# Performance work log

Measured on AMD Instinct MI355X. Metric: run time of the kernel, lower is better.

The kernel has to match this reference:

```python
import jax, jax.numpy as jnp
import numpy as np

S, V, E, H = 4096, 10000, 128, 256
NE, TK, NH, HD, FF, NL = 4, 2, 4, 64, 2048, 2
EPS = 1e-5
SCALE = 1.0 / np.sqrt(HD).astype(np.float32)


def setup_inputs() -> dict:
    key = jax.random.key(0)
    ks = iter(jax.random.split(key, 64))
    n = lambda shape: jax.random.normal(next(ks), shape, jnp.float32) * 0.02
    inp = {"x": jax.random.randint(next(ks), (S,), 0, V)}
    inp["emb"] = n((V, E))
    for i, din in enumerate([E, H, H]):
        inp[f"moe{i}_gw"] = n((NE, din))
        inp[f"moe{i}_gb"] = jnp.zeros((NE,), jnp.float32)
        inp[f"moe{i}_ew"] = n((NE, H, din))
        inp[f"moe{i}_eb"] = jnp.zeros((NE, H), jnp.float32)
    inp["attn_in_w"] = n((NL, 3 * H, H)); inp["attn_in_b"] = jnp.zeros((NL, 3 * H), jnp.float32)
    inp["attn_out_w"] = n((NL, H, H));    inp["attn_out_b"] = jnp.zeros((NL, H), jnp.float32)
    inp["ln1_g"] = jnp.ones((NL, H), jnp.float32); inp["ln1_b"] = jnp.zeros((NL, H), jnp.float32)
    inp["ln2_g"] = jnp.ones((NL, H), jnp.float32); inp["ln2_b"] = jnp.zeros((NL, H), jnp.float32)
    inp["ff1_w"] = n((NL, FF, H)); inp["ff1_b"] = jnp.zeros((NL, FF), jnp.float32)
    inp["ff2_w"] = n((NL, H, FF)); inp["ff2_b"] = jnp.zeros((NL, H), jnp.float32)
    inp["fc_w"] = n((H, H)); inp["fc_b"] = jnp.zeros((H,), jnp.float32)
    inp["out_w"] = n((V, H)); inp["out_b"] = jnp.zeros((V,), jnp.float32)
    return inp


def _ln(x, g, b):
    m = x.mean(-1, keepdims=True)
    v = ((x - m) ** 2).mean(-1, keepdims=True)
    return (x - m) * jax.lax.rsqrt(v + EPS) * g + b


def _moe(x, gw, gb, ew, eb):
    # x: [S, din]. Faithful quirk: experts are the top-k of TOKEN 0's gates,
    # applied to every token, weighted by each token's own top-k gate scores.
    scores = jax.nn.softmax(x @ gw.T + gb, axis=-1)            # [S, NE]
    vals, idx = jax.lax.top_k(scores, TK)                      # [S, TK]
    sel = idx[0]                                               # [TK]
    outs = jnp.einsum('si,khi->skh', x, ew[sel]) + eb[sel][None]  # [S, TK, H]
    return (outs * vals[:, :, None]).sum(axis=1)               # [S, H]


def reference(x, emb,
              moe0_gw, moe0_gb, moe0_ew, moe0_eb,
              moe1_gw, moe1_gb, moe1_ew, moe1_eb,
              moe2_gw, moe2_gb, moe2_ew, moe2_eb,
              attn_in_w, attn_in_b, attn_out_w, attn_out_b,
              ln1_g, ln1_b, ln2_g, ln2_b,
              ff1_w, ff1_b, ff2_w, ff2_b,
              fc_w, fc_b, out_w, out_b):
    h = emb[x]                                                 # [S, E]
    for gw, gb, ew, eb in [(moe0_gw, moe0_gb, moe0_ew, moe0_eb),
                           (moe1_gw, moe1_gb, moe1_ew, moe1_eb),
                           (moe2_gw, moe2_gb, moe2_ew, moe2_eb)]:
        h = _moe(h, gw, gb, ew, eb)                            # [S, H]
    for l in range(NL):  # post-norm TransformerEncoderLayer (relu, no dropout at eval)
        qkv = h @ attn_in_w[l].T + attn_in_b[l]                # [S, 3H]
        q, k, v = [t.reshape(S, NH, HD) for t in jnp.split(qkv, 3, axis=-1)]
        att = jax.nn.softmax(jnp.einsum('shd,thd->hst', q, k) * SCALE, axis=-1)
        a = jnp.einsum('hst,thd->shd', att, v).reshape(S, H)
        h = _ln(h + a @ attn_out_w[l].T + attn_out_b[l], ln1_g[l], ln1_b[l])
        ffh = jax.nn.relu(h @ ff1_w[l].T + ff1_b[l]) @ ff2_w[l].T + ff2_b[l]
        h = _ln(h + ffh, ln2_g[l], ln2_b[l])
    h = h @ fc_w.T + fc_b                                      # [S, H]
    logits = h @ out_w.T + out_b                               # [S, V]
    return jax.nn.log_softmax(logits, axis=-1)
```

## Files before the change

### kernel.cpp

```cpp
#include <hip/hip_runtime.h>
#include <math.h>

#define S_ 4096
#define V_ 10000
#define E_ 128
#define H_ 256
#define NE_ 4
#define NH_ 4
#define HD_ 64
#define FF_ 2048
#define NL_ 2
#define EPS_ 1e-5f
#define SCALE_ 0.125f
#define SPLITS_ 4
#define PSTRIDE_ 160

typedef __attribute__((ext_vector_type(8))) short bf16x8;
typedef __attribute__((ext_vector_type(4))) float f32x4;

static __device__ __forceinline__ short f2bf(float f) {
  unsigned u = __builtin_bit_cast(unsigned, f);
  unsigned r = (u + 0x7fffu + ((u >> 16) & 1u)) >> 16;
  return (short)r;
}
static __device__ __forceinline__ float bf2f(short s) {
  unsigned u = ((unsigned)(unsigned short)s) << 16;
  return __builtin_bit_cast(float, u);
}

struct CvtArgs {
  const float* src[9];
  short* dst[9];
  int pfx[10];
};
__global__ __launch_bounds__(256) void k_cvt(CvtArgs a, const int* __restrict__ x,
                                             const float* __restrict__ emb,
                                             short* __restrict__ h) {
  int b = blockIdx.x;
  if (b >= a.pfx[9]) {
    int i8 = (b - a.pfx[9]) * 2048 + threadIdx.x * 8;
    int s = i8 >> 7, e = i8 & 127;
    const float* sp = &emb[(size_t)x[s] * E_ + e];
    float4 v0 = *(const float4*)sp;
    float4 v1 = *(const float4*)(sp + 4);
    short4 o0, o1;
    o0.x = f2bf(v0.x); o0.y = f2bf(v0.y); o0.z = f2bf(v0.z); o0.w = f2bf(v0.w);
    o1.x = f2bf(v1.x); o1.y = f2bf(v1.y); o1.z = f2bf(v1.z); o1.w = f2bf(v1.w);
    *(short4*)&h[i8] = o0;
    *(short4*)&h[i8 + 4] = o1;
    return;
  }
  int s = 0;
  while (b >= a.pfx[s + 1]) ++s;
  size_t base = (size_t)(b - a.pfx[s]) * 2048 + threadIdx.x * 8;
  const float* sp = a.src[s] + base;
  short* dp = a.dst[s] + base;
  float4 v0 = *(const float4*)sp;
  float4 v1 = *(const float4*)(sp + 4);
  short4 o0, o1;
  o0.x = f2bf(v0.x); o0.y = f2bf(v0.y); o0.z = f2bf(v0.z); o0.w = f2bf(v0.w);
  o1.x = f2bf(v1.x); o1.y = f2bf(v1.y); o1.z = f2bf(v1.z); o1.w = f2bf(v1.w);
  *(short4*)dp = o0;
  *(short4*)(dp + 4) = o1;
}

template <int ACT>
__global__ __launch_bounds__(256) void k_gemm64(const short* __restrict__ A,
                                                const short* __restrict__ W,
                                                const float* __restrict__ bias,
                                                short* __restrict__ C,
                                                int M, int N, int K) {
  __shared__ short As[64][72];
  __shared__ short Bs[64][72];
  int bm = blockIdx.y * 64, bn = blockIdx.x * 64;
  int tid = threadIdx.x, lane = tid & 63, wv = tid >> 6;
  int quad = lane >> 4, m16 = lane & 15;
  int wr = (wv >> 1) * 32, wc = (wv & 1) * 32;
  int srow = tid >> 2, scc = (tid & 3) * 16;
  const short* Ar = A + (size_t)(bm + srow) * K + scc;
  const short* Wr = W + (size_t)(bn + srow) * K + scc;
  f32x4 acc[2][2];
#pragma unroll
  for (int m = 0; m < 2; ++m)
#pragma unroll
    for (int n = 0; n < 2; ++n) acc[m][n] = (f32x4){0.f, 0.f, 0.f, 0.f};
  for (int k0 = 0; k0 < K; k0 += 64) {
    *(bf16x8*)&As[srow][scc] = *(const bf16x8*)&Ar[k0];
    *(bf16x8*)&As[srow][scc + 8] = *(const bf16x8*)&Ar[k0 + 8];
    *(bf16x8*)&Bs[srow][scc] = *(const bf16x8*)&Wr[k0];
    *(bf16x8*)&Bs[srow][scc + 8] = *(const bf16x8*)&Wr[k0 + 8];
    __syncthreads();
#pragma unroll
    for (int kk = 0; kk < 2; ++kk) {
      bf16x8 af[2], bf[2];
#pragma unroll
      for (int m = 0; m < 2; ++m) af[m] = *(const bf16x8*)&As[wr + m * 16 + m16][kk * 32 + quad * 8];
#pragma unroll
      for (int n = 0; n < 2; ++n) bf[n] = *(const bf16x8*)&Bs[wc + n * 16 + m16][kk * 32 + quad * 8];
#pragma unroll
      for (int m = 0; m < 2; ++m)
#pragma unroll
        for (int n = 0; n < 2; ++n)
          acc[m][n] = __builtin_amdgcn_mfma_f32_16x16x32_bf16(af[m], bf[n], acc[m][n], 0, 0, 0);
    }
    __syncthreads();
  }
#pragma unroll
  for (int n = 0; n < 2; ++n) {
    int col = bn + wc + n * 16 + m16;
    float b = bias[col];
#pragma unroll
    for (int m = 0; m < 2; ++m) {
      int row0 = bm + wr + m * 16 + quad * 4;
#pragma unroll
      for (int r = 0; r < 4; ++r) {
        float v = acc[m][n][r] + b;
        if (ACT) v = fmaxf(v, 0.f);
        C[(size_t)(row0 + r) * N + col] = f2bf(v);
      }
    }
  }
}

__global__ __launch_bounds__(256) void k_proj(const float* __restrict__ Opart,
                                              const float* __restrict__ Lpart,
                                              const short* __restrict__ W,
                                              const float* __restrict__ bias,
                                              short* __restrict__ C) {
  __shared__ short As[32][40];
  __shared__ short Bs[64][40];
  int bm = blockIdx.y * 32, bn = blockIdx.x * 64;
  int tid = threadIdx.x, lane = tid & 63, wv = tid >> 6;
  int quad = lane >> 4, m16 = lane & 15;
  int wr = (wv >> 1) * 16, wc = (wv & 1) * 32;
  int srow = tid >> 2, sc = (tid & 3) * 8;
  int rowA = bm + (srow & 31);
  const short* Wr = W + (size_t)(bn + srow) * H_ + sc;
  float invden[NH_];
  if (tid < 128) {
#pragma unroll
    for (int hh = 0; hh < NH_; ++hh) {
      float dsum = 0.f;
#pragma unroll
      for (int sp = 0; sp < SPLITS_; ++sp)
        dsum += Lpart[(size_t)(sp * NH_ + hh) * S_ + rowA];
      invden[hh] = 1.0f / dsum;
    }
  }
  f32x4 acc[2];
  acc[0] = (f32x4){0.f, 0.f, 0.f, 0.f};
  acc[1] = (f32x4){0.f, 0.f, 0.f, 0.f};
#pragma unroll
  for (int k0 = 0; k0 < H_; k0 += 32) {
    if (tid < 128) {
      const int head = k0 >> 6;
      int dd = (k0 & 63) + sc;
      float n0 = 0.f, n1 = 0.f, n2 = 0.f, n3 = 0.f, n4 = 0.f, n5 = 0.f, n6 = 0.f, n7 = 0.f;
#pragma unroll
      for (int sp = 0; sp < SPLITS_; ++sp) {
        const float* op = &Opart[((size_t)(sp * NH_ + head) * S_ + rowA) * 64 + dd];
        float4 u0 = *(const float4*)op;
        float4 u1 = *(const float4*)(op + 4);
        n0 += u0.x; n1 += u0.y; n2 += u0.z; n3 += u0.w;
        n4 += u1.x; n5 += u1.y; n6 += u1.z; n7 += u1.w;
      }
      float iv = invden[head];
      union { short s[8]; bf16x8 v; } o;
      o.s[0] = f2bf(n0 * iv); o.s[1] = f2bf(n1 * iv);
      o.s[2] = f2bf(n2 * iv); o.s[3] = f2bf(n3 * iv);
      o.s[4] = f2bf(n4 * iv); o.s[5] = f2bf(n5 * iv);
      o.s[6] = f2bf(n6 * iv); o.s[7] = f2bf(n7 * iv);
      *(bf16x8*)&As[srow][sc] = o.v;
    }
    *(bf16x8*)&Bs[srow][sc] = *(const bf16x8*)&Wr[k0];
    __syncthreads();
    bf16x8 af = *(const bf16x8*)&As[wr + m16][quad * 8];
    bf16x8 bf0 = *(const bf16x8*)&Bs[wc + m16][quad * 8];
    bf16x8 bf1 = *(const bf16x8*)&Bs[wc + 16 + m16][quad * 8];
    acc[0] = __builtin_amdgcn_mfma_f32_16x16x32_bf16(af, bf0, acc[0], 0, 0, 0);
    acc[1] = __builtin_amdgcn_mfma_f32_16x16x32_bf16(af, bf1, acc[1], 0, 0, 0);
    __syncthreads();
  }
#pragma unroll
  for (int n = 0; n < 2; ++n) {
    int col = bn + wc + n * 16 + m16;
    float b = bias[col];
    int row0 = bm + wr + quad * 4;
#pragma unroll
    for (int r = 0; r < 4; ++r) {
      float v = acc[n][r] + b;
      C[(size_t)(row0 + r) * H_ + col] = f2bf(v);
    }
  }
}

__global__ __launch_bounds__(256) void k_ff2(const short* __restrict__ A,
                                             const short* __restrict__ W,
                                             const float* __restrict__ bias,
                                             short* __restrict__ C, int K) {
  __shared__ short As[32][72];
  __shared__ short Bs[64][72];
  int bm = blockIdx.y * 32, bn = blockIdx.x * 64;
  int tid = threadIdx.x, lane = tid & 63, wv = tid >> 6;
  int quad = lane >> 4, m16 = lane & 15;
  int wr = (wv >> 1) * 16, wc = (wv & 1) * 32;
  int arow = tid >> 3, ac = (tid & 7) * 8;
  int brow = tid >> 2, bc = (tid & 3) * 16;
  const short* Ar = A + (size_t)(bm + arow) * K + ac;
  const short* Wr = W + (size_t)(bn + brow) * K + bc;
  f32x4 acc[2];
  acc[0] = (f32x4){0.f, 0.f, 0.f, 0.f};
  acc[1] = (f32x4){0.f, 0.f, 0.f, 0.f};
  for (int k0 = 0; k0 < K; k0 += 64) {
    *(bf16x8*)&As[arow][ac] = *(const bf16x8*)&Ar[k0];
    *(bf16x8*)&Bs[brow][bc] = *(const bf16x8*)&Wr[k0];
    *(bf16x8*)&Bs[brow][bc + 8] = *(const bf16x8*)&Wr[k0 + 8];
    __syncthreads();
    bf16x8 af0 = *(const bf16x8*)&As[wr + m16][quad * 8];
    bf16x8 af1 = *(const bf16x8*)&As[wr + m16][32 + quad * 8];
    bf16x8 b00 = *(const bf16x8*)&Bs[wc + m16][quad * 8];
    bf16x8 b01 = *(const bf16x8*)&Bs[wc + m16][32 + quad * 8];
    bf16x8 b10 = *(const bf16x8*)&Bs[wc + 16 + m16][quad * 8];
    bf16x8 b11 = *(const bf16x8*)&Bs[wc + 16 + m16][32 + quad * 8];
    acc[0] = __builtin_amdgcn_mfma_f32_16x16x32_bf16(af0, b00, acc[0], 0, 0, 0);
    acc[0] = __builtin_amdgcn_mfma_f32_16x16x32_bf16(af1, b01, acc[0], 0, 0, 0);
    acc[1] = __builtin_amdgcn_mfma_f32_16x16x32_bf16(af0, b10, acc[1], 0, 0, 0);
    acc[1] = __builtin_amdgcn_mfma_f32_16x16x32_bf16(af1, b11, acc[1], 0, 0, 0);
    __syncthreads();
  }
#pragma unroll
  for (int n = 0; n < 2; ++n) {
    int col = bn + wc + n * 16 + m16;
    float b = bias[col];
    int row0 = bm + wr + quad * 4;
#pragma unroll
    for (int r = 0; r < 4; ++r) {
      float v = acc[n][r] + b;
      C[(size_t)(row0 + r) * H_ + col] = f2bf(v);
    }
  }
}

__global__ __launch_bounds__(256) void k_moe(const short* __restrict__ A,
                                             const short* __restrict__ EW,
                                             const float* __restrict__ EB,
                                             const float* __restrict__ gw,
                                             const float* __restrict__ gb,
                                             short* __restrict__ C,
                                             int N, int K) {
  __shared__ short As[32][40];
  __shared__ short B0s[64][40];
  __shared__ short B1s[64][40];
  __shared__ float sc_lds[32][NE_];
  __shared__ float g0_lds[NE_];
  __shared__ float vals_lds[32][2];
  __shared__ int sel_lds[2];
  int bm = blockIdx.y * 32, bn = blockIdx.x * 64;
  int tid = threadIdx.x, lane = tid & 63, wv = tid >> 6;
  int quad = lane >> 4, m16 = lane & 15;
  int wr = (wv >> 1) * 16, wc = (wv & 1) * 32;
  int srow = tid >> 2, sc = (tid & 3) * 8;
  if (tid < 128) {
    int r = tid & 31, e = tid >> 5;
    const short* xs = A + (size_t)(bm + r) * K;
    const float* w = gw + (size_t)e * K;
    float acc = 0.f;
    for (int i = 0; i < K; i += 8) {
      bf16x8 xv = *(const bf16x8*)&xs[i];
      float4 w0 = *(const float4*)&w[i];
      float4 w1 = *(const float4*)&w[i + 4];
      acc += bf2f(xv[0]) * w0.x + bf2f(xv[1]) * w0.y + bf2f(xv[2]) * w0.z + bf2f(xv[3]) * w0.w;
      acc += bf2f(xv[4]) * w1.x + bf2f(xv[5]) * w1.y + bf2f(xv[6]) * w1.z + bf2f(xv[7]) * w1.w;
    }
    sc_lds[r][e] = acc + gb[e];
  } else if (tid < 132) {
    int e = tid - 128;
    const float* w = gw + (size_t)e * K;
    float acc = 0.f;
    for (int i = 0; i < K; i += 8) {
      bf16x8 xv = *(const bf16x8*)&A[i];
      float4 w0 = *(const float4*)&w[i];
      float4 w1 = *(const float4*)&w[i + 4];
      acc += bf2f(xv[0]) * w0.x + bf2f(xv[1]) * w0.y + bf2f(xv[2]) * w0.z + bf2f(xv[3]) * w0.w;
      acc += bf2f(xv[4]) * w1.x + bf2f(xv[5]) * w1.y + bf2f(xv[6]) * w1.z + bf2f(xv[7]) * w1.w;
    }
    g0_lds[e] = acc + gb[e];
  }
  __syncthreads();
  if (tid < 32) {
    float g[4];
#pragma unroll
    for (int e = 0; e < 4; ++e) g[e] = sc_lds[tid][e];
    float mx = fmaxf(fmaxf(g[0], g[1]), fmaxf(g[2], g[3]));
    float sum = 0.f;
#pragma unroll
    for (int e = 0; e < 4; ++e) { g[e] = __expf(g[e] - mx); sum += g[e]; }
    float inv = 1.0f / sum;
#pragma unroll
    for (int e = 0; e < 4; ++e) g[e] *= inv;
    int i0 = 0; float v0 = g[0];
#pragma unroll
    for (int e = 1; e < 4; ++e) if (g[e] > v0) { v0 = g[e]; i0 = e; }
    float v1 = -1.0f;
#pragma unroll
    for (int e = 0; e < 4; ++e) if (e != i0 && g[e] > v1) v1 = g[e];
    vals_lds[tid][0] = v0;
    vals_lds[tid][1] = v1;
  } else if (tid == 32) {
    float g[4];
#pragma unroll
    for (int e = 0; e < 4; ++e) g[e] = g0_lds[e];
    float mx = fmaxf(fmaxf(g[0], g[1]), fmaxf(g[2], g[3]));
    float sum = 0.f;
#pragma unroll
    for (int e = 0; e < 4; ++e) { g[e] = __expf(g[e] - mx); sum += g[e]; }
    float inv = 1.0f / sum;
#pragma unroll
    for (int e = 0; e < 4; ++e) g[e] *= inv;
    int i0 = 0; float v0 = g[0];
#pragma unroll
    for (int e = 1; e < 4; ++e) if (g[e] > v0) { v0 = g[e]; i0 = e; }
    int i1 = 0; float v1 = -1.0f;
#pragma unroll
    for (int e = 0; e < 4; ++e) if (e != i0 && g[e] > v1) { v1 = g[e]; i1 = e; }
    sel_lds[0] = i0;
    sel_lds[1] = i1;
  }
  __syncthreads();
  int e0 = sel_lds[0], e1 = sel_lds[1];
  const short* W0r = EW + (size_t)e0 * N * K + (size_t)(bn + srow) * K + sc;
  const short* W1r = EW + (size_t)e1 * N * K + (size_t)(bn + srow) * K + sc;
  const float* b0 = EB + (size_t)e0 * N;
  const float* b1 = EB + (size_t)e1 * N;
  const short* Ar = A + (size_t)(bm + (srow & 31)) * K + sc;
  f32x4 a0[2], a1[2];
  a0[0] = a0[1] = (f32x4){0.f, 0.f, 0.f, 0.f};
  a1[0] = a1[1] = (f32x4){0.f, 0.f, 0.f, 0.f};
  for (int k0 = 0; k0 < K; k0 += 32) {
    if (tid < 128) *(bf16x8*)&As[srow][sc] = *(const bf16x8*)&Ar[k0];
    *(bf16x8*)&B0s[srow][sc] = *(const bf16x8*)&W0r[k0];
    *(bf16x8*)&B1s[srow][sc] = *(const bf16x8*)&W1r[k0];
    __syncthreads();
    bf16x8 af = *(const bf16x8*)&As[wr + m16][quad * 8];
#pragma unroll
    for (int n = 0; n < 2; ++n) {
      bf16x8 bf0 = *(const bf16x8*)&B0s[wc + n * 16 + m16][quad * 8];
      bf16x8 bf1 = *(const bf16x8*)&B1s[wc + n * 16 + m16][quad * 8];
      a0[n] = __builtin_amdgcn_mfma_f32_16x16x32_bf16(af, bf0, a0[n], 0, 0, 0);
      a1[n] = __builtin_amdgcn_mfma_f32_16x16x32_bf16(af, bf1, a1[n], 0, 0, 0);
    }
    __syncthreads();
  }
#pragma unroll
  for (int n = 0; n < 2; ++n) {
    int col = bn + wc + n * 16 + m16;
    float bb0 = b0[col], bb1 = b1[col];
    int row0 = wr + quad * 4;
#pragma unroll
    for (int r = 0; r < 4; ++r) {
      int lrow = row0 + r;
      float v = vals_lds[lrow][0] * (a0[n][r] + bb0) + vals_lds[lrow][1] * (a1[n][r] + bb1);
      C[(size_t)(bm + lrow) * N + col] = f2bf(v);
    }
  }
}

template <int ACT>
__global__ __launch_bounds__(256) void k_gemm128(const short* __restrict__ A,
                                                 const short* __restrict__ W,
                                                 const float* __restrict__ bias,
                                                 short* __restrict__ C,
                                                 int M, int N, int K) {
  __shared__ short As[128][40];
  __shared__ short Bs[128][40];
  int bm = blockIdx.y * 128, bn = blockIdx.x * 128;
  int tid = threadIdx.x, lane = tid & 63, wv = tid >> 6;
  int quad = lane >> 4, m16 = lane & 15;
  int wr = (wv >> 1) * 64, wc = (wv & 1) * 64;
  int srow = tid >> 1, sc = (tid & 1) * 16;
  const short* Ar = A + (size_t)(bm + srow) * K + sc;
  const short* Wr = W + (size_t)(bn + srow) * K + sc;
  f32x4 acc[4][4];
#pragma unroll
  for (int m = 0; m < 4; ++m)
#pragma unroll
    for (int n = 0; n < 4; ++n) acc[m][n] = (f32x4){0.f, 0.f, 0.f, 0.f};
  for (int k0 = 0; k0 < K; k0 += 32) {
    *(bf16x8*)&As[srow][sc] = *(const bf16x8*)&Ar[k0];
    *(bf16x8*)&As[srow][sc + 8] = *(const bf16x8*)&Ar[k0 + 8];
    *(bf16x8*)&Bs[srow][sc] = *(const bf16x8*)&Wr[k0];
    *(bf16x8*)&Bs[srow][sc + 8] = *(const bf16x8*)&Wr[k0 + 8];
    __syncthreads();
    bf16x8 af[4], bf[4];
#pragma unroll
    for (int m = 0; m < 4; ++m) af[m] = *(const bf16x8*)&As[wr + m * 16 + m16][quad * 8];
#pragma unroll
    for (int n = 0; n < 4; ++n) bf[n] = *(const bf16x8*)&Bs[wc + n * 16 + m16][quad * 8];
#pragma unroll
    for (int m = 0; m < 4; ++m)
#pragma unroll
      for (int n = 0; n < 4; ++n)
        acc[m][n] = __builtin_amdgcn_mfma_f32_16x16x32_bf16(af[m], bf[n], acc[m][n], 0, 0, 0);
    __syncthreads();
  }
#pragma unroll
  for (int n = 0; n < 4; ++n) {
    int col = bn + wc + n * 16 + m16;
    float b = bias[col];
#pragma unroll
    for (int m = 0; m < 4; ++m) {
      int row0 = bm + wr + m * 16 + quad * 4;
#pragma unroll
      for (int r = 0; r < 4; ++r) {
        float v = acc[m][n][r] + b;
        if (ACT) v = fmaxf(v, 0.f);
        C[(size_t)(row0 + r) * N + col] = f2bf(v);
      }
    }
  }
}

__global__ __launch_bounds__(256) void k_gsum(const short* __restrict__ A,
                                              const short* __restrict__ W,
                                              const float* __restrict__ bias,
                                              float* __restrict__ psums,
                                              int M, int N, int K) {
  __shared__ short As[128][40];
  __shared__ short Bs[128][40];
  int bm = blockIdx.y * 128, bn = blockIdx.x * 128;
  int tid = threadIdx.x, lane = tid & 63, wv = tid >> 6;
  int quad = lane >> 4, m16 = lane & 15;
  int wr = (wv >> 1) * 64, wc = (wv & 1) * 64;
  int srow = tid >> 1, sc = (tid & 1) * 16;
  const short* Ar = A + (size_t)(bm + srow) * K + sc;
  int br = bn + srow;
  const short* Wr = W + (size_t)(br < N ? br : N - 1) * K + sc;
  f32x4 acc[4][4];
#pragma unroll
  for (int m = 0; m < 4; ++m)
#pragma unroll
    for (int n = 0; n < 4; ++n) acc[m][n] = (f32x4){0.f, 0.f, 0.f, 0.f};
  for (int k0 = 0; k0 < K; k0 += 32) {
    *(bf16x8*)&As[srow][sc] = *(const bf16x8*)&Ar[k0];
    *(bf16x8*)&As[srow][sc + 8] = *(const bf16x8*)&Ar[k0 + 8];
    *(bf16x8*)&Bs[srow][sc] = *(const bf16x8*)&Wr[k0];
    *(bf16x8*)&Bs[srow][sc + 8] = *(const bf16x8*)&Wr[k0 + 8];
    __syncthreads();
    bf16x8 af[4], bf[4];
#pragma unroll
    for (int m = 0; m < 4; ++m) af[m] = *(const bf16x8*)&As[wr + m * 16 + m16][quad * 8];
#pragma unroll
    for (int n = 0; n < 4; ++n) bf[n] = *(const bf16x8*)&Bs[wc + n * 16 + m16][quad * 8];
#pragma unroll
    for (int m = 0; m < 4; ++m)
#pragma unroll
      for (int n = 0; n < 4; ++n)
        acc[m][n] = __builtin_amdgcn_mfma_f32_16x16x32_bf16(af[m], bf[n], acc[m][n], 0, 0, 0);
    __syncthreads();
  }
  float bcol[4];
  int cvalid[4];
#pragma unroll
  for (int n = 0; n < 4; ++n) {
    int col = bn + wc + n * 16 + m16;
    cvalid[n] = (col < N);
    bcol[n] = cvalid[n] ? bias[col] : 0.f;
  }
  int pslot = blockIdx.x * 2 + (wv & 1);
#pragma unroll
  for (int m = 0; m < 4; ++m) {
#pragma unroll
    for (int r = 0; r < 4; ++r) {
      int row = bm + wr + m * 16 + quad * 4 + r;
      float es = 0.f;
#pragma unroll
      for (int n = 0; n < 4; ++n) {
        if (cvalid[n]) {
          float v = acc[m][n][r] + bcol[n];
          es += __expf(v);
        }
      }
#pragma unroll
      for (int mask = 1; mask < 16; mask <<= 1) es += __shfl_xor(es, mask, 16);
      if (m16 == 0) psums[(size_t)row * PSTRIDE_ + pslot] = es;
    }
  }
}

__global__ __launch_bounds__(256) void k_lse(const float* __restrict__ psums,
                                             float* __restrict__ lse, int nslots) {
  int wv = threadIdx.x >> 6, lane = threadIdx.x & 63;
  int s = blockIdx.x * 4 + wv;
  float a = 0.f;
  for (int i = lane; i < nslots; i += 64) a += psums[(size_t)s * PSTRIDE_ + i];
#pragma unroll
  for (int mask = 1; mask < 64; mask <<= 1) a += __shfl_xor(a, mask, 64);
  if (lane == 0) lse[s] = logf(a);
}

__global__ __launch_bounds__(256) void k_gout(const short* __restrict__ A,
                                              const short* __restrict__ W,
                                              const float* __restrict__ bias,
                                              const float* __restrict__ lse,
                                              float* __restrict__ C,
                                              int M, int N, int K) {
  __shared__ short As[128][40];
  __shared__ short Bs[128][40];
  int bm = blockIdx.y * 128, bn = blockIdx.x * 128;
  int tid = threadIdx.x, lane = tid & 63, wv = tid >> 6;
  int quad = lane >> 4, m16 = lane & 15;
  int wr = (wv >> 1) * 64, wc = (wv & 1) * 64;
  int srow = tid >> 1, sc = (tid & 1) * 16;
  const short* Ar = A + (size_t)(bm + srow) * K + sc;
  int br = bn + srow;
  const short* Wr = W + (size_t)(br < N ? br : N - 1) * K + sc;
  f32x4 acc[4][4];
#pragma unroll
  for (int m = 0; m < 4; ++m)
#pragma unroll
    for (int n = 0; n < 4; ++n) acc[m][n] = (f32x4){0.f, 0.f, 0.f, 0.f};
  for (int k0 = 0; k0 < K; k0 += 32) {
    *(bf16x8*)&As[srow][sc] = *(const bf16x8*)&Ar[k0];
    *(bf16x8*)&As[srow][sc + 8] = *(const bf16x8*)&Ar[k0 + 8];
    *(bf16x8*)&Bs[srow][sc] = *(const bf16x8*)&Wr[k0];
    *(bf16x8*)&Bs[srow][sc + 8] = *(const bf16x8*)&Wr[k0 + 8];
    __syncthreads();
    bf16x8 af[4], bf[4];
#pragma unroll
    for (int m = 0; m < 4; ++m) af[m] = *(const bf16x8*)&As[wr + m * 16 + m16][quad * 8];
#pragma unroll
    for (int n = 0; n < 4; ++n) bf[n] = *(const bf16x8*)&Bs[wc + n * 16 + m16][quad * 8];
#pragma unroll
    for (int m = 0; m < 4; ++m)
#pragma unroll
      for (int n = 0; n < 4; ++n)
        acc[m][n] = __builtin_amdgcn_mfma_f32_16x16x32_bf16(af[m], bf[n], acc[m][n], 0, 0, 0);
    __syncthreads();
  }
  float bcol[4];
  int cvalid[4];
#pragma unroll
  for (int n = 0; n < 4; ++n) {
    int col = bn + wc + n * 16 + m16;
    cvalid[n] = (col < N);
    bcol[n] = cvalid[n] ? bias[col] : 0.f;
  }
#pragma unroll
  for (int m = 0; m < 4; ++m) {
#pragma unroll
    for (int r = 0; r < 4; ++r) {
      int row = bm + wr + m * 16 + quad * 4 + r;
      float flse = lse[row];
#pragma unroll
      for (int n = 0; n < 4; ++n) {
        if (cvalid[n]) {
          float v = acc[m][n][r] + bcol[n] - flse;
          C[(size_t)row * N + (bn + wc + n * 16 + m16)] = v;
        }
      }
    }
  }
}

__global__ __launch_bounds__(256) void k_attn(const short* __restrict__ qkv,
                                              float* __restrict__ Opart,
                                              float* __restrict__ Lpart) {
  __shared__ short Ks[64][72];
  __shared__ short Vt[64][72];
  int tid = threadIdx.x, lane = tid & 63, wv = tid >> 6;
  int quad = lane >> 4, m16 = lane & 15;
  int head = blockIdx.y, hd0 = head * HD_;
  int split = blockIdx.z;
  int qbaseA = blockIdx.x * 128 + wv * 16;
  int qbaseB = qbaseA + 64;
  bf16x8 qfA[2], qfB[2];
  {
    const short* qrA = qkv + (size_t)(qbaseA + m16) * (3 * H_) + hd0 + quad * 8;
    qfA[0] = *(const bf16x8*)&qrA[0];
    qfA[1] = *(const bf16x8*)&qrA[32];
    const short* qrB = qkv + (size_t)(qbaseB + m16) * (3 * H_) + hd0 + quad * 8;
    qfB[0] = *(const bf16x8*)&qrB[0];
    qfB[1] = *(const bf16x8*)&qrB[32];
  }
  f32x4 oA[4], oB[4];
#pragma unroll
  for (int dt = 0; dt < 4; ++dt) {
    oA[dt] = (f32x4){0.f, 0.f, 0.f, 0.f};
    oB[dt] = (f32x4){0.f, 0.f, 0.f, 0.f};
  }
  float lA = 0.f, lB = 0.f;

  int kb_end = (split + 1) * (S_ / 64 / SPLITS_);
  for (int kb = split * (S_ / 64 / SPLITS_); kb < kb_end; ++kb) {
    __syncthreads();
    {
      int key = tid >> 2, d0 = (tid & 3) * 16;
      const short* kr = qkv + (size_t)(kb * 64 + key) * (3 * H_) + H_ + hd0 + d0;
      *(bf16x8*)&Ks[key][d0] = *(const bf16x8*)&kr[0];
      *(bf16x8*)&Ks[key][d0 + 8] = *(const bf16x8*)&kr[8];
    }
    {
      int key0 = (tid & 15) * 4, d0 = (tid >> 4) * 4;
      const short* vbase = qkv + (size_t)(kb * 64 + key0) * (3 * H_) + 2 * H_ + hd0 + d0;
      short4 v0 = *(const short4*)&vbase[0];
      short4 v1 = *(const short4*)&vbase[3 * H_];
      short4 v2 = *(const short4*)&vbase[6 * H_];
      short4 v3 = *(const short4*)&vbase[9 * H_];
      short4 t0 = {v0.x, v1.x, v2.x, v3.x};
      short4 t1 = {v0.y, v1.y, v2.y, v3.y};
      short4 t2 = {v0.z, v1.z, v2.z, v3.z};
      short4 t3 = {v0.w, v1.w, v2.w, v3.w};
      *(short4*)&Vt[d0 + 0][key0] = t0;
      *(short4*)&Vt[d0 + 1][key0] = t1;
      *(short4*)&Vt[d0 + 2][key0] = t2;
      *(short4*)&Vt[d0 + 3][key0] = t3;
    }
    __syncthreads();
    f32x4 sA[4], sB[4];
#pragma unroll
    for (int kt = 0; kt < 4; ++kt) {
      bf16x8 ak0 = *(const bf16x8*)&Ks[kt * 16 + m16][quad * 8];
      bf16x8 ak1 = *(const bf16x8*)&Ks[kt * 16 + m16][32 + quad * 8];
      f32x4 zA = (f32x4){0.f, 0.f, 0.f, 0.f};
      zA = __builtin_amdgcn_mfma_f32_16x16x32_bf16(ak0, qfA[0], zA, 0, 0, 0);
      zA = __builtin_amdgcn_mfma_f32_16x16x32_bf16(ak1, qfA[1], zA, 0, 0, 0);
      sA[kt] = zA;
      f32x4 zB = (f32x4){0.f, 0.f, 0.f, 0.f};
      zB = __builtin_amdgcn_mfma_f32_16x16x32_bf16(ak0, qfB[0], zB, 0, 0, 0);
      zB = __builtin_amdgcn_mfma_f32_16x16x32_bf16(ak1, qfB[1], zB, 0, 0, 0);
      sB[kt] = zB;
    }
    unsigned pwA[4][2], pwB[4][2];
    {
      float rsum = 0.f;
#pragma unroll
      for (int kt = 0; kt < 4; ++kt) {
        float p0 = __expf(sA[kt][0] * SCALE_);
        float p1 = __expf(sA[kt][1] * SCALE_);
        float p2 = __expf(sA[kt][2] * SCALE_);
        float p3 = __expf(sA[kt][3] * SCALE_);
        rsum += (p0 + p1) + (p2 + p3);
        asm("v_cvt_pk_bf16_f32 %0, %1, %2" : "=v"(pwA[kt][0]) : "v"(p0), "v"(p1));
        asm("v_cvt_pk_bf16_f32 %0, %1, %2" : "=v"(pwA[kt][1]) : "v"(p2), "v"(p3));
      }
      unsigned ua = __builtin_bit_cast(unsigned, rsum), ub = ua;
      asm volatile("v_permlane16_swap_b32 %0, %1" : "+v"(ua), "+v"(ub));
      float s01 = __builtin_bit_cast(float, ua) + __builtin_bit_cast(float, ub);
      unsigned uc = __builtin_bit_cast(unsigned, s01), ud = uc;
      asm volatile("v_permlane32_swap_b32 %0, %1" : "+v"(uc), "+v"(ud));
      lA += __builtin_bit_cast(float, uc) + __builtin_bit_cast(float, ud);
    }
    {
      float rsum = 0.f;
#pragma unroll
      for (int kt = 0; kt < 4; ++kt) {
        float p0 = __expf(sB[kt][0] * SCALE_);
        float p1 = __expf(sB[kt][1] * SCALE_);
        float p2 = __expf(sB[kt][2] * SCALE_);
        float p3 = __expf(sB[kt][3] * SCALE_);
        rsum += (p0 + p1) + (p2 + p3);
        asm("v_cvt_pk_bf16_f32 %0, %1, %2" : "=v"(pwB[kt][0]) : "v"(p0), "v"(p1));
        asm("v_cvt_pk_bf16_f32 %0, %1, %2" : "=v"(pwB[kt][1]) : "v"(p2), "v"(p3));
      }
      unsigned ua = __builtin_bit_cast(unsigned, rsum), ub = ua;
      asm volatile("v_permlane16_swap_b32 %0, %1" : "+v"(ua), "+v"(ub));
      float s01 = __builtin_bit_cast(float, ua) + __builtin_bit_cast(float, ub);
      unsigned uc = __builtin_bit_cast(unsigned, s01), ud = uc;
      asm volatile("v_permlane32_swap_b32 %0, %1" : "+v"(uc), "+v"(ud));
      lB += __builtin_bit_cast(float, uc) + __builtin_bit_cast(float, ud);
    }
#pragma unroll
    for (int c = 0; c < 2; ++c) {
      unsigned a0 = pwA[2 * c][0], b0 = pwA[2 * c + 1][0];
      asm volatile("v_permlane32_swap_b32 %0, %1" : "+v"(a0), "+v"(b0));
      asm volatile("v_permlane16_swap_b32 %0, %1" : "+v"(a0), "+v"(b0));
      unsigned a1 = pwA[2 * c][1], b1 = pwA[2 * c + 1][1];
      asm volatile("v_permlane32_swap_b32 %0, %1" : "+v"(a1), "+v"(b1));
      asm volatile("v_permlane16_swap_b32 %0, %1" : "+v"(a1), "+v"(b1));
      union { unsigned u[4]; bf16x8 v; } puA;
      puA.u[0] = a0; puA.u[1] = a1; puA.u[2] = b0; puA.u[3] = b1;
      bf16x8 paA = puA.v;
      unsigned c0 = pwB[2 * c][0], d0w = pwB[2 * c + 1][0];
      asm volatile("v_permlane32_swap_b32 %0, %1" : "+v"(c0), "+v"(d0w));
      asm volatile("v_permlane16_swap_b32 %0, %1" : "+v"(c0), "+v"(d0w));
      unsigned c1 = pwB[2 * c][1], d1w = pwB[2 * c + 1][1];
      asm volatile("v_permlane32_swap_b32 %0, %1" : "+v"(c1), "+v"(d1w));
      asm volatile("v_permlane16_swap_b32 %0, %1" : "+v"(c1), "+v"(d1w));
      union { unsigned u[4]; bf16x8 v; } puB;
      puB.u[0] = c0; puB.u[1] = c1; puB.u[2] = d0w; puB.u[3] = d1w;
      bf16x8 paB = puB.v;
#pragma unroll
      for (int dt = 0; dt < 4; ++dt) {
        bf16x8 bv = *(const bf16x8*)&Vt[dt * 16 + m16][c * 32 + quad * 8];
        oA[dt] = __builtin_amdgcn_mfma_f32_16x16x32_bf16(paA, bv, oA[dt], 0, 0, 0);
        oB[dt] = __builtin_amdgcn_mfma_f32_16x16x32_bf16(paB, bv, oB[dt], 0, 0, 0);
      }
    }
  }
  float* Op = Opart + ((size_t)(split * NH_ + head) * S_) * 64;
#pragma unroll
  for (int dt = 0; dt < 4; ++dt) {
#pragma unroll
    for (int r = 0; r < 4; ++r) {
      int rowA = qbaseA + quad * 4 + r;
      Op[(size_t)rowA * 64 + dt * 16 + m16] = oA[dt][r];
      int rowB = qbaseB + quad * 4 + r;
      Op[(size_t)rowB * 64 + dt * 16 + m16] = oB[dt][r];
    }
  }
  if (quad == 0) {
    float* Lp = Lpart + (size_t)(split * NH_ + head) * S_;
    Lp[qbaseA + m16] = lA;
    Lp[qbaseB + m16] = lB;
  }
}

__global__ __launch_bounds__(256) void k_add_ln(short* __restrict__ h,
                                                const short* __restrict__ t_,
                                                const float* __restrict__ g,
                                                const float* __restrict__ b) {
  int wv = threadIdx.x >> 6, lane = threadIdx.x & 63;
  int s = blockIdx.x * 4 + wv;
  size_t off = (size_t)s * H_ + lane * 4;
  short4 hv = *(const short4*)&h[off];
  short4 tv = *(const short4*)&t_[off];
  float x[4] = {bf2f(hv.x) + bf2f(tv.x), bf2f(hv.y) + bf2f(tv.y),
                bf2f(hv.z) + bf2f(tv.z), bf2f(hv.w) + bf2f(tv.w)};
  float sum = x[0] + x[1] + x[2] + x[3];
#pragma unroll
  for (int mask = 1; mask < 64; mask <<= 1) sum += __shfl_xor(sum, mask, 64);
  float mean = sum * (1.0f / H_);
  float d[4], vs = 0.f;
#pragma unroll
  for (int i = 0; i < 4; ++i) { d[i] = x[i] - mean; vs += d[i] * d[i]; }
#pragma unroll
  for (int mask = 1; mask < 64; mask <<= 1) vs += __shfl_xor(vs, mask, 64);
  float inv = rsqrtf(vs * (1.0f / H_) + EPS_);
  float4 gv = *(const float4*)&g[lane * 4];
  float4 bv = *(const float4*)&b[lane * 4];
  short4 ov;
  ov.x = f2bf(d[0] * inv * gv.x + bv.x);
  ov.y = f2bf(d[1] * inv * gv.y + bv.y);
  ov.z = f2bf(d[2] * inv * gv.z + bv.z);
  ov.w = f2bf(d[3] * inv * gv.w + bv.w);
  *(short4*)&h[off] = ov;
}

extern "C" void kernel_launch(void* const* d_in, const int* in_sizes, int n_in,
                              void* d_out, int out_size, void* d_ws, size_t ws_size,
                              hipStream_t stream) {
  const int* x = (const int*)d_in[0];
  const float* emb = (const float*)d_in[1];
  const float* moe_gw[3] = {(const float*)d_in[2], (const float*)d_in[6], (const float*)d_in[10]};
  const float* moe_gb[3] = {(const float*)d_in[3], (const float*)d_in[7], (const float*)d_in[11]};
  const float* moe_eb[3] = {(const float*)d_in[5], (const float*)d_in[9], (const float*)d_in[13]};
  const float* attn_in_b = (const float*)d_in[15];
  const float* attn_out_b = (const float*)d_in[17];
  const float* ln1_g = (const float*)d_in[18];
  const float* ln1_b = (const float*)d_in[19];
  const float* ln2_g = (const float*)d_in[20];
  const float* ln2_b = (const float*)d_in[21];
  const float* ff1_b = (const float*)d_in[23];
  const float* ff2_b = (const float*)d_in[25];
  const float* fc_b = (const float*)d_in[27];
  const float* out_b = (const float*)d_in[29];
  float* out = (float*)d_out;

  short* wsS = (short*)d_ws;
  size_t off = 0;
  auto alloc = [&](size_t n) { short* p = wsS + off; off += n; return p; };
  short* ewb0 = alloc(131072);
  short* ewb1 = alloc(262144);
  short* ewb2 = alloc(262144);
  short* aiwb = alloc(393216);
  short* aowb = alloc(131072);
  short* f1wb = alloc(1048576);
  short* f2wb = alloc(1048576);
  short* fcwb = alloc(65536);
  short* owb  = alloc(2560000);
  short* hb_e = alloc((size_t)S_ * E_);
  short* hb_a = alloc((size_t)S_ * H_);
  short* hb_b = alloc((size_t)S_ * H_);
  short* qkvb = alloc((size_t)S_ * 3 * H_);
  short* abufb = alloc((size_t)S_ * H_);
  short* tmpb = alloc((size_t)S_ * H_);
  short* ffhb = alloc((size_t)S_ * FF_);
  float* Opart = (float*)ffhb;
  float* Lpart = (float*)tmpb;
  float* psums = (float*)f1wb;
  float* lse = psums + (size_t)S_ * PSTRIDE_;

  const short* moe_ewb[3] = {ewb0, ewb1, ewb2};

  CvtArgs ca;
  ca.src[0] = (const float*)d_in[4];  ca.dst[0] = ewb0;
  ca.src[1] = (const float*)d_in[8];  ca.dst[1] = ewb1;
  ca.src[2] = (const float*)d_in[12]; ca.dst[2] = ewb2;
  ca.src[3] = (const float*)d_in[14]; ca.dst[3] = aiwb;
  ca.src[4] = (const float*)d_in[16]; ca.dst[4] = aowb;
  ca.src[5] = (const float*)d_in[22]; ca.dst[5] = f1wb;
  ca.src[6] = (const float*)d_in[24]; ca.dst[6] = f2wb;
  ca.src[7] = (const float*)d_in[26]; ca.dst[7] = fcwb;
  ca.src[8] = (const float*)d_in[28]; ca.dst[8] = owb;
  int sizes[9] = {131072, 262144, 262144, 393216, 131072, 1048576, 1048576, 65536, 2560000};
  ca.pfx[0] = 0;
  for (int i = 0; i < 9; ++i) ca.pfx[i + 1] = ca.pfx[i] + sizes[i] / 2048;
  k_cvt<<<dim3(ca.pfx[9] + S_ * E_ / 2048), dim3(256), 0, stream>>>(ca, x, emb, hb_e);

  const short* moe_in[3] = {hb_e, hb_a, hb_b};
  short* moe_out[3] = {hb_a, hb_b, hb_a};
  int moe_k[3] = {E_, H_, H_};
  for (int i = 0; i < 3; ++i) {
    k_moe<<<dim3(H_ / 64, S_ / 32), dim3(256), 0, stream>>>(
        moe_in[i], moe_ewb[i], moe_eb[i], moe_gw[i], moe_gb[i], moe_out[i], H_, moe_k[i]);
  }

  for (int l = 0; l < NL_; ++l) {
    k_gemm64<0><<<dim3(3 * H_ / 64, S_ / 64), dim3(256), 0, stream>>>(
        hb_a, aiwb + (size_t)l * 3 * H_ * H_, attn_in_b + (size_t)l * 3 * H_, qkvb, S_, 3 * H_, H_);
    k_attn<<<dim3(S_ / 128, NH_, SPLITS_), dim3(256), 0, stream>>>(qkvb, Opart, Lpart);
    k_proj<<<dim3(H_ / 64, S_ / 32), dim3(256), 0, stream>>>(
        Opart, Lpart, aowb + (size_t)l * H_ * H_, attn_out_b + (size_t)l * H_, tmpb);
    k_add_ln<<<dim3(S_ / 4), dim3(256), 0, stream>>>(hb_a, tmpb, ln1_g + l * H_, ln1_b + l * H_);
    k_gemm128<1><<<dim3(FF_ / 128, S_ / 128), dim3(256), 0, stream>>>(
        hb_a, f1wb + (size_t)l * FF_ * H_, ff1_b + (size_t)l * FF_, ffhb, S_, FF_, H_);
    k_ff2<<<dim3(H_ / 64, S_ / 32), dim3(256), 0, stream>>>(
        ffhb, f2wb + (size_t)l * H_ * FF_, ff2_b + (size_t)l * H_, tmpb, FF_);
    k_add_ln<<<dim3(S_ / 4), dim3(256), 0, stream>>>(hb_a, tmpb, ln2_g + l * H_, ln2_b + l * H_);
  }

  k_ff2<<<dim3(H_ / 64, S_ / 32), dim3(256), 0, stream>>>(hb_a, fcwb, fc_b, tmpb, H_);
  int nxb = (V_ + 127) / 128;
  k_gsum<<<dim3(nxb, S_ / 128), dim3(256), 0, stream>>>(tmpb, owb, out_b, psums, S_, V_, H_);
  k_lse<<<dim3(S_ / 4), dim3(256), 0, stream>>>(psums, lse, nxb * 2);
  k_gout<<<dim3(nxb, S_ / 128), dim3(256), 0, stream>>>(tmpb, owb, out_b, lse, out, S_, V_, H_);
}
```

Baseline: 587.3 us.

## Fuse residual add and LayerNorm into attention-proj and FF2 GEMM epilogues

Replaces the attention output projection and FF2 GEMMs with full-row (32x256) tile kernels that add the residual, apply bias, and compute LayerNorm in the epilogue via cross-wave shared-memory reductions. This drops the tmp buffer round trip and four k_add_ln launches per forward pass. In exchange, the grid shrinks to 128 blocks (from 512), which lowers parallelism on a GPU with many CUs. The FF2 K=2048 loop now has each block reload the full 256-row weight slice.

Result: slower. 601.0 us (+2.3%).

```diff
diff --git a/kernel.cpp b/kernel.cpp
--- a/kernel.cpp
+++ b/kernel.cpp
@@ -122,76 +122,254 @@
   }
 }
 
-__global__ __launch_bounds__(256) void k_proj(const float* __restrict__ Opart,
-                                              const float* __restrict__ Lpart,
-                                              const short* __restrict__ W,
-                                              const float* __restrict__ bias,
-                                              short* __restrict__ C) {
-  __shared__ short As[32][40];
-  __shared__ short Bs[64][40];
-  int bm = blockIdx.y * 32, bn = blockIdx.x * 64;
+__global__ __launch_bounds__(256) void k_projln(const float* __restrict__ Opart,
+                                                const float* __restrict__ Lpart,
+                                                const short* __restrict__ W,
+                                                const float* __restrict__ bias,
+                                                short* __restrict__ h,
+                                                const float* __restrict__ g,
+                                                const float* __restrict__ b) {
+  __shared__ short As[32][72];
+  __shared__ short Bs[256][72];
+  __shared__ float red[32][4];
+  int bm = blockIdx.x * 32;
   int tid = threadIdx.x, lane = tid & 63, wv = tid >> 6;
   int quad = lane >> 4, m16 = lane & 15;
-  int wr = (wv >> 1) * 16, wc = (wv & 1) * 32;
-  int srow = tid >> 2, sc = (tid & 3) * 8;
-  int rowA = bm + (srow & 31);
-  const short* Wr = W + (size_t)(bn + srow) * H_ + sc;
+  int wc = wv * 64;
+  int arow = tid >> 3, ac = (tid & 7) * 8;
   float invden[NH_];
-  if (tid < 128) {
-#pragma unroll
-    for (int hh = 0; hh < NH_; ++hh) {
-      float dsum = 0.f;
-#pragma unroll
-      for (int sp = 0; sp < SPLITS_; ++sp)
-        dsum += Lpart[(size_t)(sp * NH_ + hh) * S_ + rowA];
-      invden[hh] = 1.0f / dsum;
-    }
-  }
-  f32x4 acc[2];
-  acc[0] = (f32x4){0.f, 0.f, 0.f, 0.f};
-  acc[1] = (f32x4){0.f, 0.f, 0.f, 0.f};
-#pragma unroll
-  for (int k0 = 0; k0 < H_; k0 += 32) {
-    if (tid < 128) {
+#pragma unroll
+  for (int hh = 0; hh < NH_; ++hh) {
+    float dsum = 0.f;
+#pragma unroll
+    for (int sp = 0; sp < SPLITS_; ++sp)
+      dsum += Lpart[(size_t)(sp * NH_ + hh) * S_ + bm + arow];
+    invden[hh] = 1.0f / dsum;
+  }
+  f32x4 acc[2][4];
+#pragma unroll
+  for (int m = 0; m < 2; ++m)
+#pragma unroll
+    for (int n = 0; n < 4; ++n) acc[m][n] = (f32x4){0.f, 0.f, 0.f, 0.f};
+#pragma unroll
+  for (int k0 = 0; k0 < H_; k0 += 64) {
+    {
       const int head = k0 >> 6;
-      int dd = (k0 & 63) + sc;
-      float n0 = 0.f, n1 = 0.f, n2 = 0.f, n3 = 0.f, n4 = 0.f, n5 = 0.f, n6 = 0.f, n7 = 0.f;
+      int rowA = bm + arow;
+      float ns[8] = {0.f, 0.f, 0.f, 0.f, 0.f, 0.f, 0.f, 0.f};
 #pragma unroll
       for (int sp = 0; sp < SPLITS_; ++sp) {
-        const float* op = &Opart[((size_t)(sp * NH_ + head) * S_ + rowA) * 64 + dd];
+        const float* op = &Opart[((size_t)(sp * NH_ + head) * S_ + rowA) * 64 + ac];
         float4 u0 = *(const float4*)op;
         float4 u1 = *(const float4*)(op + 4);
-        n0 += u0.x; n1 += u0.y; n2 += u0.z; n3 += u0.w;
-        n4 += u1.x; n5 += u1.y; n6 += u1.z; n7 += u1.w;
+        ns[0] += u0.x; ns[1] += u0.y; ns[2] += u0.z; ns[3] += u0.w;
+        ns[4] += u1.x; ns[5] += u1.y; ns[6] += u1.z; ns[7] += u1.w;
       }
       float iv = invden[head];
       union { short s[8]; bf16x8 v; } o;
-      o.s[0] = f2bf(n0 * iv); o.s[1] = f2bf(n1 * iv);
-      o.s[2] = f2bf(n2 * iv); o.s[3] = f2bf(n3 * iv);
-      o.s[4] = f2bf(n4 * iv); o.s[5] = f2bf(n5 * iv);
-      o.s[6] = f2bf(n6 * iv); o.s[7] = f2bf(n7 * iv);
-      *(bf16x8*)&As[srow][sc] = o.v;
-    }
-    *(bf16x8*)&Bs[srow][sc] = *(const bf16x8*)&Wr[k0];
-    __syncthreads();
-    bf16x8 af = *(const bf16x8*)&As[wr + m16][quad * 8];
-    bf16x8 bf0 = *(const bf16x8*)&Bs[wc + m16][quad * 8];
-    bf16x8 bf1 = *(const bf16x8*)&Bs[wc + 16 + m16][quad * 8];
-    acc[0] = __builtin_amdgcn_mfma_f32_16x16x32_bf16(af, bf0, acc[0], 0, 0, 0);
-    acc[1] = __builtin_amdgcn_mfma_f32_16x16x32_bf16(af, bf1, acc[1], 0, 0, 0);
-    __syncthreads();
-  }
-#pragma unroll
-  for (int n = 0; n < 2; ++n) {
-    int col = bn + wc + n * 16 + m16;
-    float b = bias[col];
-    int row0 = bm + wr + quad * 4;
-#pragma unroll
-    for (int r = 0; r < 4; ++r) {
-      float v = acc[n][r] + b;
-      C[(size_t)(row0 + r) * H_ + col] = f2bf(v);
-    }
-  }
+#pragma unroll
+      for (int j = 0; j < 8; ++j) o.s[j] = f2bf(ns[j] * iv);
+      *(bf16x8*)&As[arow][ac] = o.v;
+    }
+#pragma unroll
+    for (int p = 0; p < 4; ++p) {
+      int br = p * 64 + (tid >> 2), bc = (tid & 3) * 16;
+      const short* wp = &W[(size_t)br * H_ + k0 + bc];
+      *(bf16x8*)&Bs[br][bc] = *(const bf16x8*)&wp[0];
+      *(bf16x8*)&Bs[br][bc + 8] = *(const bf16x8*)&wp[8];
+    }
+    __syncthreads();
+#pragma unroll
+    for (int kk = 0; kk < 2; ++kk) {
+      bf16x8 af[2], bf[4];
+#pragma unroll
+      for (int m = 0; m < 2; ++m) af[m] = *(const bf16x8*)&As[m * 16 + m16][kk * 32 + quad * 8];
+#pragma unroll
+      for (int n = 0; n < 4; ++n) bf[n] = *(const bf16x8*)&Bs[wc + n * 16 + m16][kk * 32 + quad * 8];
+#pragma unroll
+      for (int m = 0; m < 2; ++m)
+#pragma unroll
+        for (int n = 0; n < 4; ++n)
+          acc[m][n] = __builtin_amdgcn_mfma_f32_16x16x32_bf16(af[m], bf[n], acc[m][n], 0, 0, 0);
+    }
+    __syncthreads();
+  }
+  float bcol[4], gcol[4], bbcol[4];
+  int col[4];
+#pragma unroll
+  for (int n = 0; n < 4; ++n) {
+    col[n] = wc + n * 16 + m16;
+    bcol[n] = bias[col[n]];
+    gcol[n] = g[col[n]];
+    bbcol[n] = b[col[n]];
+  }
+  float x[2][4][4];
+#pragma unroll
+  for (int m = 0; m < 2; ++m)
+#pragma unroll
+    for (int r = 0; r < 4; ++r) {
+      int row = bm + m * 16 + quad * 4 + r;
+#pragma unroll
+      for (int n = 0; n < 4; ++n)
+        x[m][n][r] = bf2f(h[(size_t)row * H_ + col[n]]) + acc[m][n][r] + bcol[n];
+    }
+#pragma unroll
+  for (int m = 0; m < 2; ++m)
+#pragma unroll
+    for (int r = 0; r < 4; ++r) {
+      float s = (x[m][0][r] + x[m][1][r]) + (x[m][2][r] + x[m][3][r]);
+#pragma unroll
+      for (int mask = 1; mask < 16; mask <<= 1) s += __shfl_xor(s, mask, 16);
+      if (m16 == 0) red[m * 16 + quad * 4 + r][wv] = s;
+    }
+  __syncthreads();
+  float mean[2][4];
+#pragma unroll
+  for (int m = 0; m < 2; ++m)
+#pragma unroll
+    for (int r = 0; r < 4; ++r) {
+      int R = m * 16 + quad * 4 + r;
+      mean[m][r] = (red[R][0] + red[R][1] + red[R][2] + red[R][3]) * (1.0f / H_);
+    }
+  __syncthreads();
+#pragma unroll
+  for (int m = 0; m < 2; ++m)
+#pragma unroll
+    for (int r = 0; r < 4; ++r) {
+      float s = 0.f;
+#pragma unroll
+      for (int n = 0; n < 4; ++n) { float d = x[m][n][r] - mean[m][r]; s += d * d; }
+#pragma unroll
+      for (int mask = 1; mask < 16; mask <<= 1) s += __shfl_xor(s, mask, 16);
+      if (m16 == 0) red[m * 16 + quad * 4 + r][wv] = s;
+    }
+  __syncthreads();
+#pragma unroll
+  for (int m = 0; m < 2; ++m)
+#pragma unroll
+    for (int r = 0; r < 4; ++r) {
+      int R = m * 16 + quad * 4 + r;
+      float var = (red[R][0] + red[R][1] + red[R][2] + red[R][3]) * (1.0f / H_);
+      float inv = rsqrtf(var + EPS_);
+      int row = bm + R;
+#pragma unroll
+      for (int n = 0; n < 4; ++n) {
+        float v = (x[m][n][r] - mean[m][r]) * inv * gcol[n] + bbcol[n];
+        h[(size_t)row * H_ + col[n]] = f2bf(v);
+      }
+    }
+}
+
+__global__ __launch_bounds__(256) void k_ff2ln(const short* __restrict__ A,
+                                               const short* __restrict__ W,
+                                               const float* __restrict__ bias,
+                                               short* __restrict__ h,
+                                               const float* __restrict__ g,
+                                               const float* __restrict__ b,
+                                               int K) {
+  __shared__ short As[32][72];
+  __shared__ short Bs[256][72];
+  __shared__ float red[32][4];
+  int bm = blockIdx.x * 32;
+  int tid = threadIdx.x, lane = tid & 63, wv = tid >> 6;
+  int quad = lane >> 4, m16 = lane & 15;
+  int wc = wv * 64;
+  int arow = tid >> 3, ac = (tid & 7) * 8;
+  const short* Ar = A + (size_t)(bm + arow) * K + ac;
+  f32x4 acc[2][4];
+#pragma unroll
+  for (int m = 0; m < 2; ++m)
+#pragma unroll
+    for (int n = 0; n < 4; ++n) acc[m][n] = (f32x4){0.f, 0.f, 0.f, 0.f};
+  for (int k0 = 0; k0 < K; k0 += 64) {
+    *(bf16x8*)&As[arow][ac] = *(const bf16x8*)&Ar[k0];
+#pragma unroll
+    for (int p = 0; p < 4; ++p) {
+      int br = p * 64 + (tid >> 2), bc = (tid & 3) * 16;
+      const short* wp = &W[(size_t)br * K + k0 + bc];
+      *(bf16x8*)&Bs[br][bc] = *(const bf16x8*)&wp[0];
+      *(bf16x8*)&Bs[br][bc + 8] = *(const bf16x8*)&wp[8];
+    }
+    __syncthreads();
+#pragma unroll
+    for (int kk = 0; kk < 2; ++kk) {
+      bf16x8 af[2], bf[4];
+#pragma unroll
+      for (int m = 0; m < 2; ++m) af[m] = *(const bf16x8*)&As[m * 16 + m16][kk * 32 + quad * 8];
+#pragma unroll
+      for (int n = 0; n < 4; ++n) bf[n] = *(const bf16x8*)&Bs[wc + n * 16 + m16][kk * 32 + quad * 8];
+#pragma unroll
+      for (int m = 0; m < 2; ++m)
+#pragma unroll
+        for (int n = 0; n < 4; ++n)
+          acc[m][n] = __builtin_amdgcn_mfma_f32_16x16x32_bf16(af[m], bf[n], acc[m][n], 0, 0, 0);
+    }
+    __syncthreads();
+  }
+  float bcol[4], gcol[4], bbcol[4];
+  int col[4];
+#pragma unroll
+  for (int n = 0; n < 4; ++n) {
+    col[n] = wc + n * 16 + m16;
+    bcol[n] = bias[col[n]];
+    gcol[n] = g[col[n]];
+    bbcol[n] = b[col[n]];
+  }
+  float x[2][4][4];
+#pragma unroll
+  for (int m = 0; m < 2; ++m)
+#pragma unroll
+    for (int r = 0; r < 4; ++r) {
+      int row = bm + m * 16 + quad * 4 + r;
+#pragma unroll
+      for (int n = 0; n < 4; ++n)
+        x[m][n][r] = bf2f(h[(size_t)row * H_ + col[n]]) + acc[m][n][r] + bcol[n];
+    }
+#pragma unroll
+  for (int m = 0; m < 2; ++m)
+#pragma unroll
+    for (int r = 0; r < 4; ++r) {
+      float s = (x[m][0][r] + x[m][1][r]) + (x[m][2][r] + x[m][3][r]);
+#pragma unroll
+      for (int mask = 1; mask < 16; mask <<= 1) s += __shfl_xor(s, mask, 16);
+      if (m16 == 0) red[m * 16 + quad * 4 + r][wv] = s;
+    }
+  __syncthreads();
+  float mean[2][4];
+#pragma unroll
+  for (int m = 0; m < 2; ++m)
+#pragma unroll
+    for (int r = 0; r < 4; ++r) {
+      int R = m * 16 + quad * 4 + r;
+      mean[m][r] = (red[R][0] + red[R][1] + red[R][2] + red[R][3]) * (1.0f / H_);
+    }
+  __syncthreads();
+#pragma unroll
+  for (int m = 0; m < 2; ++m)
+#pragma unroll
+    for (int r = 0; r < 4; ++r) {
+      float s = 0.f;
+#pragma unroll
+      for (int n = 0; n < 4; ++n) { float d = x[m][n][r] - mean[m][r]; s += d * d; }
+#pragma unroll
+      for (int mask = 1; mask < 16; mask <<= 1) s += __shfl_xor(s, mask, 16);
+      if (m16 == 0) red[m * 16 + quad * 4 + r][wv] = s;
+    }
+  __syncthreads();
+#pragma unroll
+  for (int m = 0; m < 2; ++m)
+#pragma unroll
+    for (int r = 0; r < 4; ++r) {
+      int R = m * 16 + quad * 4 + r;
+      float var = (red[R][0] + red[R][1] + red[R][2] + red[R][3]) * (1.0f / H_);
+      float inv = rsqrtf(var + EPS_);
+      int row = bm + R;
+#pragma unroll
+      for (int n = 0; n < 4; ++n) {
+        float v = (x[m][n][r] - mean[m][r]) * inv * gcol[n] + bbcol[n];
+        h[(size_t)row * H_ + col[n]] = f2bf(v);
+      }
+    }
 }
 
 __global__ __launch_bounds__(256) void k_ff2(const short* __restrict__ A,
@@ -715,37 +893,6 @@
   }
 }
 
-__global__ __launch_bounds__(256) void k_add_ln(short* __restrict__ h,
-                                                const short* __restrict__ t_,
-                                                const float* __restrict__ g,
-                                                const float* __restrict__ b) {
-  int wv = threadIdx.x >> 6, lane = threadIdx.x & 63;
-  int s = blockIdx.x * 4 + wv;
-  size_t off = (size_t)s * H_ + lane * 4;
-  short4 hv = *(const short4*)&h[off];
-  short4 tv = *(const short4*)&t_[off];
-  float x[4] = {bf2f(hv.x) + bf2f(tv.x), bf2f(hv.y) + bf2f(tv.y),
-                bf2f(hv.z) + bf2f(tv.z), bf2f(hv.w) + bf2f(tv.w)};
-  float sum = x[0] + x[1] + x[2] + x[3];
-#pragma unroll
-  for (int mask = 1; mask < 64; mask <<= 1) sum += __shfl_xor(sum, mask, 64);
-  float mean = sum * (1.0f / H_);
-  float d[4], vs = 0.f;
-#pragma unroll
-  for (int i = 0; i < 4; ++i) { d[i] = x[i] - mean; vs += d[i] * d[i]; }
-#pragma unroll
-  for (int mask = 1; mask < 64; mask <<= 1) vs += __shfl_xor(vs, mask, 64);
-  float inv = rsqrtf(vs * (1.0f / H_) + EPS_);
-  float4 gv = *(const float4*)&g[lane * 4];
-  float4 bv = *(const float4*)&b[lane * 4];
-  short4 ov;
-  ov.x = f2bf(d[0] * inv * gv.x + bv.x);
-  ov.y = f2bf(d[1] * inv * gv.y + bv.y);
-  ov.z = f2bf(d[2] * inv * gv.z + bv.z);
-  ov.w = f2bf(d[3] * inv * gv.w + bv.w);
-  *(short4*)&h[off] = ov;
-}
-
 extern "C" void kernel_launch(void* const* d_in, const int* in_sizes, int n_in,
                               void* d_out, int out_size, void* d_ws, size_t ws_size,
                               hipStream_t stream) {
@@ -819,14 +966,14 @@
     k_gemm64<0><<<dim3(3 * H_ / 64, S_ / 64), dim3(256), 0, stream>>>(
         hb_a, aiwb + (size_t)l * 3 * H_ * H_, attn_in_b + (size_t)l * 3 * H_, qkvb, S_, 3 * H_, H_);
     k_attn<<<dim3(S_ / 128, NH_, SPLITS_), dim3(256), 0, stream>>>(qkvb, Opart, Lpart);
-    k_proj<<<dim3(H_ / 64, S_ / 32), dim3(256), 0, stream>>>(
-        Opart, Lpart, aowb + (size_t)l * H_ * H_, attn_out_b + (size_t)l * H_, tmpb);
-    k_add_ln<<<dim3(S_ / 4), dim3(256), 0, stream>>>(hb_a, tmpb, ln1_g + l * H_, ln1_b + l * H_);
+    k_projln<<<dim3(S_ / 32), dim3(256), 0, stream>>>(
+        Opart, Lpart, aowb + (size_t)l * H_ * H_, attn_out_b + (size_t)l * H_,
+        hb_a, ln1_g + l * H_, ln1_b + l * H_);
     k_gemm128<1><<<dim3(FF_ / 128, S_ / 128), dim3(256), 0, stream>>>(
         hb_a, f1wb + (size_t)l * FF_ * H_, ff1_b + (size_t)l * FF_, ffhb, S_, FF_, H_);
-    k_ff2<<<dim3(H_ / 64, S_ / 32), dim3(256), 0, stream>>>(
-        ffhb, f2wb + (size_t)l * H_ * FF_, ff2_b + (size_t)l * H_, tmpb, FF_);
-    k_add_ln<<<dim3(S_ / 4), dim3(256), 0, stream>>>(hb_a, tmpb, ln2_g + l * H_, ln2_b + l * H_);
+    k_ff2ln<<<dim3(S_ / 32), dim3(256), 0, stream>>>(
+        ffhb, f2wb + (size_t)l * H_ * FF_, ff2_b + (size_t)l * H_,
+        hb_a, ln2_g + l * H_, ln2_b + l * H_, FF_);
   }
 
   k_ff2<<<dim3(H_ / 64, S_ / 32), dim3(256), 0, stream>>>(hb_a, fcwb, fc_b, tmpb, H_);
```
